# Kernel optimization log

Hardware: AMD Instinct MI355X
Metric: run time of the kernel (lower is better)

The kernel has to match this reference:

```python
import jax, jax.numpy as jnp
import numpy as np


def setup_inputs() -> dict:
    key = jax.random.key(0)
    k0, k1, k2, k3 = jax.random.split(key, 4)
    B, N, D, C, F = 8192, 784, 64, 10, 2  # batch, input_dim, bond_dim, num_classes, feature_dim
    x = jax.random.uniform(k0, (B, N), dtype=jnp.float32)  # pixel values in [0,1]
    core0 = jax.random.normal(k1, (F, 1, D), dtype=jnp.float32) * 0.1
    base = jnp.broadcast_to(jnp.eye(D, dtype=jnp.float32), (N - 2, F, D, D))
    cores_mid = base + jax.random.normal(k2, (N - 2, F, D, D), dtype=jnp.float32) * 0.01
    core_last = jax.random.normal(k3, (F, D, C), dtype=jnp.float32) * 0.1
    return {"x": x, "core0": core0, "cores_mid": cores_mid, "core_last": core_last}


def reference(x, core0, cores_mid, core_last):
    EPS = 1e-8
    factor = jnp.float32(np.pi / 2.0)
    # FeatureMap: [B, N] -> [B, N, 2] with (cos, sin)
    feats = jnp.stack([jnp.cos(factor * x), jnp.sin(factor * x)], axis=-1)
    # First site: M = v0 @ A0.squeeze(1)  -> [B, D]
    M = jnp.einsum('bf,fd->bd', feats[:, 0, :], core0[:, 0, :])
    # Sequential left->right contraction over middle sites with per-step L2 normalization
    v_mid = jnp.moveaxis(feats[:, 1:-1, :], 1, 0)  # [N-2, B, 2]

    def step(M, inp):
        v, A = inp  # v: [B, 2], A: [2, D, D]
        Mn = jnp.einsum('bi,bf,fij->bj', M, v, A)
        Mn = Mn / (jnp.linalg.norm(Mn, axis=1, keepdims=True) + EPS)
        return Mn, None

    M, _ = jax.lax.scan(step, M, (v_mid, cores_mid))
    # Last site: logits[b,c] = sum_i M[b,i] * (v_N[b,f] A_N[f,i,c])
    logits = jnp.einsum('bi,bf,fic->bc', M, feats[:, -1, :], core_last)
    return logits
```

## Files before the change

### kernel.cpp

```cpp
#include <hip/hip_runtime.h>

typedef __attribute__((ext_vector_type(8))) short s16x8;
typedef __attribute__((ext_vector_type(4))) float f32x4;
typedef __attribute__((ext_vector_type(4))) int i32x4;

#define NMID 782
#define PI_2 1.5707963267948966f
#define EG_STEP_BYTES 16384
#define EG_ELEMS ((size_t)NMID * 8192)
#define SLAB_B 4352

__device__ __forceinline__ int cvt_pk_bf16(float a, float b) {
  int r;
  asm("v_cvt_pk_bf16_f32 %0, %1, %2" : "=v"(r) : "v"(a), "v"(b));
  return r;
}

__device__ __forceinline__ f32x4 mfma_bf16(i32x4 a, i32x4 b, f32x4 c) {
  return __builtin_amdgcn_mfma_f32_16x16x32_bf16(
      __builtin_bit_cast(s16x8, a), __builtin_bit_cast(s16x8, b), c, 0, 0, 0);
}

__device__ __forceinline__ unsigned short bf16_rne(float v) {
  unsigned u = __float_as_uint(v);
  return (unsigned short)((u + 0x7FFFu + ((u >> 16) & 1)) >> 16);
}

__global__ __launch_bounds__(256) void prep_eg(const float* __restrict__ cm,
                                               unsigned short* __restrict__ eg) {
  const int n = blockIdx.x;
  const float* src = cm + (size_t)n * 8192;
  unsigned short* dst = eg + (size_t)n * 8192;
#pragma unroll
  for (int it = 0; it < 4; ++it) {
    int row = it * 256 + threadIdx.x;
    int q = row >> 6, l = row & 63;
    int t = q >> 2, cc = q & 3;
    int f = cc >> 1, c2 = cc & 1, h = l >> 4;
    int j = 16 * t + (l & 15);
    unsigned short v8[8];
#pragma unroll
    for (int e = 0; e < 8; ++e) {
      int i = 32 * c2 + 16 * (e >> 2) + 4 * h + (e & 3);
      float val = src[(f * 64 + i) * 64 + j] - (i == j ? 1.0f : 0.0f);
      v8[e] = bf16_rne(val);
    }
    *(uint4*)(dst + (size_t)row * 8) = *(const uint4*)v8;
  }
}

#define STEP4(nc, CUR, NXT, CC, SS)                                          \
  {                                                                          \
    int np = (nc) + 3;                                                       \
    if (np >= NMID) np = NMID - 1;                                           \
    const char* pnxt = base + (size_t)np * EG_STEP_BYTES;                    \
    _Pragma("unroll") for (int q = 0; q < 4; ++q)                            \
        NXT[q] = *(const i32x4*)(pnxt + q * 1024);                           \
    int b0[4], b1[4];                                                        \
    _Pragma("unroll") for (int p = 0; p < 4; ++p) {                          \
      b0[p] = cvt_pk_bf16(fm[2 * p], fm[2 * p + 1]);                         \
      b1[p] = cvt_pk_bf16(fm[8 + 2 * p], fm[8 + 2 * p + 1]);                 \
    }                                                                        \
    i32x4 B0 = {b0[0], b0[1], b0[2], b0[3]};                                 \
    i32x4 B1 = {b1[0], b1[1], b1[2], b1[3]};                                 \
    float cps = (CC) + (SS);                                                 \
    f32x4 z = {0.f, 0.f, 0.f, 0.f};                                          \
    f32x4 accA = mfma_bf16(CUR[0], B0, z);                                   \
    accA = mfma_bf16(CUR[1], B1, accA);                                      \
    f32x4 accB = mfma_bf16(CUR[2], B0, z);                                   \
    accB = mfma_bf16(CUR[3], B1, accB);                                      \
    f32x4 mn;                                                                \
    _Pragma("unroll") for (int r = 0; r < 4; ++r)                            \
        mn[r] = cps * own4[r] + (CC)*accA[r] + (SS)*accB[r];                 \
    char* wslab = xlds + ((nc)&1) * SLAB_B;                                  \
    *(f32x4*)(wslab + bl * 272 + wcol) = mn;                                 \
    asm volatile("s_waitcnt lgkmcnt(0)" ::: "memory");                       \
    __builtin_amdgcn_s_barrier();                                            \
    __builtin_amdgcn_sched_barrier(0);                                       \
    _Pragma("unroll") for (int tp = 0; tp < 4; ++tp) {                       \
      f32x4 v = *(const f32x4*)(wslab + bl * 272 + tp * 64 + 16 * h);        \
      _Pragma("unroll") for (int r = 0; r < 4; ++r) fm[tp * 4 + r] = v[r];   \
    }                                                                        \
    own4 = *(const f32x4*)(wslab + bl * 272 + wcol);                         \
  }

__global__ __launch_bounds__(256) void mps_main(
    const float* __restrict__ x, const float* __restrict__ core0,
    const float* __restrict__ core_last, const unsigned short* __restrict__ eg,
    float* __restrict__ out) {
  __shared__ alignas(16) char xlds[2 * SLAB_B];
  const int lane = threadIdx.x & 63;
  const int wv = threadIdx.x >> 6;
  const int bl = lane & 15;
  const int h = lane >> 4;
  const int b = blockIdx.x * 16 + bl;
  const float* xr = x + (size_t)b * 784;
  const int wcol = 64 * wv + 16 * h;
  const char* base = (const char*)eg + (size_t)wv * 4096 + (size_t)lane * 16;

  float fm[16];
  f32x4 own4;
  {
    float xv = xr[0];
    float s, c;
    __sincosf(PI_2 * xv, &s, &c);
#pragma unroll
    for (int t = 0; t < 4; ++t)
#pragma unroll
      for (int r = 0; r < 4; ++r) {
        int j = 16 * t + 4 * h + r;
        fm[t * 4 + r] = c * core0[j] + s * core0[64 + j];
      }
#pragma unroll
    for (int r = 0; r < 4; ++r) {
      int j = 16 * wv + 4 * h + r;
      own4[r] = c * core0[j] + s * core0[64 + j];
    }
  }

  i32x4 frA[4], frB[4], frC[4], frD[4];
#pragma unroll
  for (int q = 0; q < 4; ++q)
    frA[q] = *(const i32x4*)(base + 0 * EG_STEP_BYTES + q * 1024);
#pragma unroll
  for (int q = 0; q < 4; ++q)
    frB[q] = *(const i32x4*)(base + 1 * EG_STEP_BYTES + q * 1024);
#pragma unroll
  for (int q = 0; q < 4; ++q)
    frC[q] = *(const i32x4*)(base + 2 * EG_STEP_BYTES + q * 1024);

  float xq[12], xqn[12];
  *(f32x4*)&xq[0] = *(const f32x4*)(xr + 0);
  *(f32x4*)&xq[4] = *(const f32x4*)(xr + 4);
  *(f32x4*)&xq[8] = *(const f32x4*)(xr + 8);

  for (int g = 0; g < 97; ++g) {
    if (g < 96) {
      const float* xp = xr + 8 * (g + 1);
      *(f32x4*)&xqn[0] = *(const f32x4*)(xp + 0);
      *(f32x4*)&xqn[4] = *(const f32x4*)(xp + 4);
      *(f32x4*)&xqn[8] = *(const f32x4*)(xp + 8);
    } else {
      *(f32x4*)&xqn[0] = *(const f32x4*)(xr + 776);
      *(f32x4*)&xqn[4] = *(const f32x4*)(xr + 780);
    }

    float cg[8], sg[8];
#pragma unroll
    for (int k = 0; k < 8; ++k) __sincosf(PI_2 * xq[1 + k], &sg[k], &cg[k]);

    if ((g & 7) == 0) {
      float ss = 0.f;
#pragma unroll
      for (int i = 0; i < 16; ++i) ss += fm[i] * fm[i];
      ss += __shfl_xor(ss, 16);
      ss += __shfl_xor(ss, 32);
      float inv = rsqrtf(ss);
#pragma unroll
      for (int i = 0; i < 16; ++i) fm[i] *= inv;
#pragma unroll
      for (int r = 0; r < 4; ++r) own4[r] *= inv;
    }

    int n0 = 8 * g;
    STEP4(n0 + 0, frA, frD, cg[0], sg[0]);
    STEP4(n0 + 1, frB, frA, cg[1], sg[1]);
    STEP4(n0 + 2, frC, frB, cg[2], sg[2]);
    STEP4(n0 + 3, frD, frC, cg[3], sg[3]);
    STEP4(n0 + 4, frA, frD, cg[4], sg[4]);
    STEP4(n0 + 5, frB, frA, cg[5], sg[5]);
    STEP4(n0 + 6, frC, frB, cg[6], sg[6]);
    STEP4(n0 + 7, frD, frC, cg[7], sg[7]);

#pragma unroll
    for (int i = 0; i < 12; ++i) xq[i] = xqn[i];
  }

  {
    float cg[6], sg[6];
#pragma unroll
    for (int k = 0; k < 6; ++k) __sincosf(PI_2 * xq[1 + k], &sg[k], &cg[k]);
    STEP4(776, frA, frD, cg[0], sg[0]);
    STEP4(777, frB, frA, cg[1], sg[1]);
    STEP4(778, frC, frB, cg[2], sg[2]);
    STEP4(779, frD, frC, cg[3], sg[3]);
    STEP4(780, frA, frD, cg[4], sg[4]);
    STEP4(781, frB, frA, cg[5], sg[5]);
  }

  float ss = 0.f;
#pragma unroll
  for (int i = 0; i < 16; ++i) ss += fm[i] * fm[i];
  ss += __shfl_xor(ss, 16);
  ss += __shfl_xor(ss, 32);
  float inv = 1.0f / (sqrtf(ss) + 1e-8f);
#pragma unroll
  for (int i = 0; i < 16; ++i) fm[i] *= inv;

  float xv = xq[7];
  float s, c;
  __sincosf(PI_2 * xv, &s, &c);
  float part[10];
#pragma unroll
  for (int cc = 0; cc < 10; ++cc) part[cc] = 0.f;
#pragma unroll
  for (int t = 0; t < 4; ++t)
#pragma unroll
    for (int r = 0; r < 4; ++r) {
      int i = 16 * t + 4 * h + r;
      float mv = fm[t * 4 + r];
#pragma unroll
      for (int cc = 0; cc < 10; ++cc)
        part[cc] += mv * (c * core_last[i * 10 + cc] + s * core_last[640 + i * 10 + cc]);
    }
#pragma unroll
  for (int cc = 0; cc < 10; ++cc) {
    part[cc] += __shfl_xor(part[cc], 16);
    part[cc] += __shfl_xor(part[cc], 32);
  }
  if (wv == 0 && h == 0) {
#pragma unroll
    for (int cc = 0; cc < 10; ++cc) out[b * 10 + cc] = part[cc];
  }
}

__global__ __launch_bounds__(64) void mps_slow(const float* __restrict__ x,
                                               const float* __restrict__ core0,
                                               const float* __restrict__ cm,
                                               const float* __restrict__ cl,
                                               float* __restrict__ out) {
  int b = blockIdx.x * 64 + threadIdx.x;
  float m[64], mn[64];
  float s, c;
  __sincosf(PI_2 * x[(size_t)b * 784], &s, &c);
  for (int d = 0; d < 64; ++d) m[d] = c * core0[d] + s * core0[64 + d];
  for (int n = 0; n < NMID; ++n) {
    __sincosf(PI_2 * x[(size_t)b * 784 + n + 1], &s, &c);
    const float* A0 = cm + (size_t)n * 8192;
    const float* A1 = A0 + 4096;
    for (int j = 0; j < 64; ++j) mn[j] = 0.f;
    for (int i = 0; i < 64; ++i) {
      float w0 = c * m[i], w1 = s * m[i];
      for (int j = 0; j < 64; ++j) mn[j] += w0 * A0[i * 64 + j] + w1 * A1[i * 64 + j];
    }
    float ssn = 0.f;
    for (int j = 0; j < 64; ++j) ssn += mn[j] * mn[j];
    float inv = 1.f / (sqrtf(ssn) + 1e-8f);
    for (int j = 0; j < 64; ++j) m[j] = mn[j] * inv;
  }
  __sincosf(PI_2 * x[(size_t)b * 784 + 783], &s, &c);
  for (int cc = 0; cc < 10; ++cc) {
    float acc = 0.f;
    for (int i = 0; i < 64; ++i)
      acc += m[i] * (c * cl[i * 10 + cc] + s * cl[640 + i * 10 + cc]);
    out[b * 10 + cc] = acc;
  }
}

extern "C" void kernel_launch(void* const* d_in, const int* in_sizes, int n_in,
                              void* d_out, int out_size, void* d_ws, size_t ws_size,
                              hipStream_t stream) {
  const float* x = (const float*)d_in[0];
  const float* core0 = (const float*)d_in[1];
  const float* cm = (const float*)d_in[2];
  const float* cl = (const float*)d_in[3];
  float* out = (float*)d_out;
  size_t need = EG_ELEMS * sizeof(unsigned short);
  if (ws_size >= need) {
    unsigned short* eg = (unsigned short*)d_ws;
    prep_eg<<<NMID, 256, 0, stream>>>(cm, eg);
    mps_main<<<512, 256, 0, stream>>>(x, core0, cl, eg, out);
  } else {
    mps_slow<<<8192 / 64, 64, 0, stream>>>(x, core0, cm, cl, out);
  }
}
```

Measured before the change: 301.0 us.

## Exchange bf16-packed MFMA operands through LDS instead of fp32 state

Each step now converts its new state slice to packed bf16 and writes it straight into LDS in B-operand layout. After the barrier, threads read the ready B0/B1 fragments with two 16-byte loads, replacing five fp32 loads and per-step conversion. The periodic renormalization computes the norm from the bf16 operands and folds the scale into the next step's cos/sin coefficients instead of rescaling registers. This shrinks LDS traffic and slab size and trims register and VALU work on the serial critical path. The trade-off is that the norm is now taken from bf16-rounded values, and a final fp32 gather through LDS is added.

```diff
diff --git a/kernel.cpp b/kernel.cpp
--- a/kernel.cpp
+++ b/kernel.cpp
@@ -8,7 +8,7 @@
 #define PI_2 1.5707963267948966f
 #define EG_STEP_BYTES 16384
 #define EG_ELEMS ((size_t)NMID * 8192)
-#define SLAB_B 4352
+#define SLAB_B 2304
 
 __device__ __forceinline__ int cvt_pk_bf16(float a, float b) {
   int r;
@@ -49,39 +49,37 @@
   }
 }
 
-#define STEP4(nc, CUR, NXT, CC, SS)                                          \
-  {                                                                          \
-    int np = (nc) + 3;                                                       \
-    if (np >= NMID) np = NMID - 1;                                           \
-    const char* pnxt = base + (size_t)np * EG_STEP_BYTES;                    \
-    _Pragma("unroll") for (int q = 0; q < 4; ++q)                            \
-        NXT[q] = *(const i32x4*)(pnxt + q * 1024);                           \
-    int b0[4], b1[4];                                                        \
-    _Pragma("unroll") for (int p = 0; p < 4; ++p) {                          \
-      b0[p] = cvt_pk_bf16(fm[2 * p], fm[2 * p + 1]);                         \
-      b1[p] = cvt_pk_bf16(fm[8 + 2 * p], fm[8 + 2 * p + 1]);                 \
-    }                                                                        \
-    i32x4 B0 = {b0[0], b0[1], b0[2], b0[3]};                                 \
-    i32x4 B1 = {b1[0], b1[1], b1[2], b1[3]};                                 \
-    float cps = (CC) + (SS);                                                 \
-    f32x4 z = {0.f, 0.f, 0.f, 0.f};                                          \
-    f32x4 accA = mfma_bf16(CUR[0], B0, z);                                   \
-    accA = mfma_bf16(CUR[1], B1, accA);                                      \
-    f32x4 accB = mfma_bf16(CUR[2], B0, z);                                   \
-    accB = mfma_bf16(CUR[3], B1, accB);                                      \
-    f32x4 mn;                                                                \
-    _Pragma("unroll") for (int r = 0; r < 4; ++r)                            \
-        mn[r] = cps * own4[r] + (CC)*accA[r] + (SS)*accB[r];                 \
-    char* wslab = xlds + ((nc)&1) * SLAB_B;                                  \
-    *(f32x4*)(wslab + bl * 272 + wcol) = mn;                                 \
-    asm volatile("s_waitcnt lgkmcnt(0)" ::: "memory");                       \
-    __builtin_amdgcn_s_barrier();                                            \
-    __builtin_amdgcn_sched_barrier(0);                                       \
-    _Pragma("unroll") for (int tp = 0; tp < 4; ++tp) {                       \
-      f32x4 v = *(const f32x4*)(wslab + bl * 272 + tp * 64 + 16 * h);        \
-      _Pragma("unroll") for (int r = 0; r < 4; ++r) fm[tp * 4 + r] = v[r];   \
-    }                                                                        \
-    own4 = *(const f32x4*)(wslab + bl * 272 + wcol);                         \
+#define STEP4(nc, CUR, NXT, CC, SS)                                         \
+  {                                                                         \
+    int np = (nc) + 3;                                                      \
+    if (np >= NMID) np = NMID - 1;                                          \
+    const char* pnxt = base + (size_t)np * EG_STEP_BYTES;                   \
+    _Pragma("unroll") for (int q = 0; q < 4; ++q)                           \
+        NXT[q] = *(const i32x4*)(pnxt + q * 1024);                          \
+    float cps = (CC) + (SS);                                                \
+    f32x4 z = {0.f, 0.f, 0.f, 0.f};                                         \
+    f32x4 accA = mfma_bf16(CUR[0], B0, z);                                  \
+    accA = mfma_bf16(CUR[1], B1, accA);                                     \
+    f32x4 accB = mfma_bf16(CUR[2], B0, z);                                  \
+    accB = mfma_bf16(CUR[3], B1, accB);                                     \
+    f32x4 mn;                                                               \
+    _Pragma("unroll") for (int r = 0; r < 4; ++r)                           \
+        mn[r] = cps * own4[r] + (CC)*accA[r] + (SS)*accB[r];                \
+    own4 = mn;                                                              \
+    int2 wq;                                                                \
+    wq.x = cvt_pk_bf16(mn[0], mn[1]);                                       \
+    wq.y = cvt_pk_bf16(mn[2], mn[3]);                                       \
+    *(int2*)(xlds + (((nc) + 1) & 1) * SLAB_B + bl * 144 + h * 32 +         \
+             wv * 8) = wq;                                                  \
+    asm volatile("s_waitcnt lgkmcnt(0)" ::: "memory");                      \
+    __builtin_amdgcn_s_barrier();                                           \
+    __builtin_amdgcn_sched_barrier(0);                                      \
+    {                                                                       \
+      const char* rb =                                                      \
+          xlds + (((nc) + 1) & 1) * SLAB_B + bl * 144 + h * 32;             \
+      B0 = *(const i32x4*)(rb);                                             \
+      B1 = *(const i32x4*)(rb + 16);                                        \
+    }                                                                       \
   }
 
 __global__ __launch_bounds__(256) void mps_main(
@@ -95,15 +93,15 @@
   const int h = lane >> 4;
   const int b = blockIdx.x * 16 + bl;
   const float* xr = x + (size_t)b * 784;
-  const int wcol = 64 * wv + 16 * h;
   const char* base = (const char*)eg + (size_t)wv * 4096 + (size_t)lane * 16;
 
-  float fm[16];
   f32x4 own4;
+  i32x4 B0, B1;
   {
     float xv = xr[0];
     float s, c;
     __sincosf(PI_2 * xv, &s, &c);
+    float fm[16];
 #pragma unroll
     for (int t = 0; t < 4; ++t)
 #pragma unroll
@@ -112,9 +110,11 @@
         fm[t * 4 + r] = c * core0[j] + s * core0[64 + j];
       }
 #pragma unroll
-    for (int r = 0; r < 4; ++r) {
-      int j = 16 * wv + 4 * h + r;
-      own4[r] = c * core0[j] + s * core0[64 + j];
+    for (int r = 0; r < 4; ++r) own4[r] = fm[wv * 4 + r];
+#pragma unroll
+    for (int p = 0; p < 4; ++p) {
+      B0[p] = cvt_pk_bf16(fm[2 * p], fm[2 * p + 1]);
+      B1[p] = cvt_pk_bf16(fm[8 + 2 * p], fm[8 + 2 * p + 1]);
     }
   }
 
@@ -152,14 +152,19 @@
     if ((g & 7) == 0) {
       float ss = 0.f;
 #pragma unroll
-      for (int i = 0; i < 16; ++i) ss += fm[i] * fm[i];
+      for (int p = 0; p < 4; ++p) {
+        unsigned u0 = (unsigned)B0[p], u1 = (unsigned)B1[p];
+        float a0 = __uint_as_float(u0 << 16);
+        float a1 = __uint_as_float(u0 & 0xFFFF0000u);
+        float b0f = __uint_as_float(u1 << 16);
+        float b1f = __uint_as_float(u1 & 0xFFFF0000u);
+        ss += a0 * a0 + a1 * a1 + b0f * b0f + b1f * b1f;
+      }
       ss += __shfl_xor(ss, 16);
       ss += __shfl_xor(ss, 32);
       float inv = rsqrtf(ss);
-#pragma unroll
-      for (int i = 0; i < 16; ++i) fm[i] *= inv;
-#pragma unroll
-      for (int r = 0; r < 4; ++r) own4[r] *= inv;
+      cg[0] *= inv;
+      sg[0] *= inv;
     }
 
     int n0 = 8 * g;
@@ -186,6 +191,20 @@
     STEP4(779, frD, frC, cg[3], sg[3]);
     STEP4(780, frA, frD, cg[4], sg[4]);
     STEP4(781, frB, frA, cg[5], sg[5]);
+  }
+
+  asm volatile("s_waitcnt lgkmcnt(0)" ::: "memory");
+  __builtin_amdgcn_s_barrier();
+  *(f32x4*)(xlds + wv * 1152 + lane * 16) = own4;
+  asm volatile("s_waitcnt lgkmcnt(0)" ::: "memory");
+  __builtin_amdgcn_s_barrier();
+  __builtin_amdgcn_sched_barrier(0);
+  float fm[16];
+#pragma unroll
+  for (int t = 0; t < 4; ++t) {
+    f32x4 v = *(const f32x4*)(xlds + t * 1152 + lane * 16);
+#pragma unroll
+    for (int r = 0; r < 4; ++r) fm[t * 4 + r] = v[r];
   }
 
   float ss = 0.f;
```

Result: faster. 267.9 us (-11.0%).
